# Kernel optimization log

Measured on AMD Instinct MI355X. Metric: run time of the kernel, lower is better.

The kernel has to match this reference:

```python
import jax, jax.numpy as jnp
import numpy as np

N_HEADS = 16
D_MODEL = 1024
D_HEAD = 64
MAX_SEQ_LEN = 1024


def setup_inputs() -> dict:
    key = jax.random.key(0)
    ks = jax.random.split(key, 7)
    std = np.sqrt(2.0 / (D_MODEL + D_HEAD)).astype(np.float32)
    hd = N_HEADS * D_HEAD
    # Weights stored as (in, out) so projection is x @ W (torch Linear y = x W^T).
    Wq = jax.random.normal(ks[0], (D_MODEL, hd), jnp.float32) * std
    Wk = jax.random.normal(ks[1], (D_MODEL, hd), jnp.float32) * std
    Wv = jax.random.normal(ks[2], (D_MODEL, hd), jnp.float32) * std
    Wo = jax.random.normal(ks[3], (hd, D_MODEL), jnp.float32) * (1.0 / np.sqrt(hd))
    bo = jnp.zeros((D_MODEL,), jnp.float32)
    rel_pos_bias = jax.random.normal(ks[4], (N_HEADS, MAX_SEQ_LEN), jnp.float32) * 0.02
    x = jax.random.normal(ks[5], (4, 1024, D_MODEL), jnp.float32)
    return {"x": x, "Wq": Wq, "Wk": Wk, "Wv": Wv, "Wo": Wo, "bo": bo,
            "rel_pos_bias": rel_pos_bias}


def _pos_bias(rel_pos_bias, T):
    # bias[h, i, j] = rel_pos_bias[h, MAX_SEQ_LEN - 1 - (i - j)] for j <= i, else 0
    i = jnp.arange(T)[:, None]
    j = jnp.arange(T)[None, :]
    idx = jnp.clip(MAX_SEQ_LEN - 1 - (i - j), 0, MAX_SEQ_LEN - 1)
    bias = rel_pos_bias[:, idx]                      # [H, T, T]
    return jnp.where((j <= i)[None], bias, 0.0)


def reference(x, Wq, Wk, Wv, Wo, bo, rel_pos_bias):
    B, T, _ = x.shape
    H, dh = N_HEADS, D_HEAD
    q = (x @ Wq).reshape(B, T, H, dh).transpose(0, 2, 1, 3)  # [B,H,T,dh]
    k = (x @ Wk).reshape(B, T, H, dh).transpose(0, 2, 1, 3)
    v = (x @ Wv).reshape(B, T, H, dh).transpose(0, 2, 1, 3)
    logits = jnp.einsum('bhqd,bhkd->bhqk', q, k)
    i = jnp.arange(T)[:, None]
    j = jnp.arange(T)[None, :]
    causal = jnp.where(j > i, -jnp.inf, 0.0)                 # [T,T]
    logits = logits + causal[None, None] + _pos_bias(rel_pos_bias, T)[None]
    logits = logits / dh                                     # note: /d_head, not sqrt
    probs = jax.nn.softmax(logits, axis=-1)
    out = jnp.einsum('bhqk,bhkd->bhqd', probs, v)            # [B,H,T,dh]
    out = out.transpose(0, 2, 1, 3).reshape(B, T, H * dh)
    return out @ Wo + bo
```

## Files before the change

kernel.cpp:

```cpp
#include <hip/hip_runtime.h>
#include <math.h>

#define BATCH 4
#define SEQ   1024
#define DM    1024
#define NH    16
#define DH    64
#define BT    (BATCH*SEQ)

typedef _Float16 f16x8 __attribute__((ext_vector_type(8)));
typedef _Float16 f16x4 __attribute__((ext_vector_type(4)));
typedef float    f32x4 __attribute__((ext_vector_type(4)));

#define GLL16(ldsdst, gsrc) \
  __builtin_amdgcn_global_load_lds((const __attribute__((address_space(1))) void*)(gsrc), \
                                   (__attribute__((address_space(3))) void*)(ldsdst), 16, 0, 0)

__global__ __launch_bounds__(256) void cvt_x(const float* __restrict__ x,
                                             _Float16* __restrict__ xh, int nquads)
{
    int i = blockIdx.x * blockDim.x + threadIdx.x;
    for (; i < nquads; i += gridDim.x * blockDim.x) {
        float4 f = ((const float4*)x)[i];
        f16x4 h;
        h[0] = (_Float16)f.x; h[1] = (_Float16)f.y;
        h[2] = (_Float16)f.z; h[3] = (_Float16)f.w;
        ((f16x4*)xh)[i] = h;
    }
}

__global__ __launch_bounds__(256) void cvt_wT(
    const float* __restrict__ W0, const float* __restrict__ W1,
    const float* __restrict__ W2, const float* __restrict__ W3,
    _Float16* __restrict__ T0, _Float16* __restrict__ T1,
    _Float16* __restrict__ T2, _Float16* __restrict__ T3)
{
    __shared__ _Float16 tile[64][72];
    const int z = blockIdx.z;
    const float* W = (z == 0) ? W0 : (z == 1) ? W1 : (z == 2) ? W2 : W3;
    _Float16*    T = (z == 0) ? T0 : (z == 1) ? T1 : (z == 2) ? T2 : T3;
    const int n0 = blockIdx.x * 64;
    const int k0 = blockIdx.y * 64;
    const int tid = threadIdx.x;
#pragma unroll
    for (int p = 0; p < 4; ++p) {
        int r = (tid >> 4) + p * 16;
        int c = (tid & 15) * 4;
        float4 f = *(const float4*)&W[(size_t)(k0 + r) * DM + n0 + c];
        f16x4 h;
        h[0] = (_Float16)f.x; h[1] = (_Float16)f.y;
        h[2] = (_Float16)f.z; h[3] = (_Float16)f.w;
        *(f16x4*)&tile[r][c] = h;
    }
    __syncthreads();
#pragma unroll
    for (int p = 0; p < 2; ++p) {
        int nr = (tid >> 3) + p * 32;
        int kc = (tid & 7) * 8;
        f16x8 vv;
#pragma unroll
        for (int i = 0; i < 8; ++i) vv[i] = tile[kc + i][nr];
        *(f16x8*)&T[(size_t)(n0 + nr) * DM + k0 + kc] = vv;
    }
}

template<int MODE>
__global__ __launch_bounds__(256) void gemm_mfma(
    const _Float16* __restrict__ A,
    const _Float16* __restrict__ B0, const _Float16* __restrict__ B1,
    const _Float16* __restrict__ B2,
    void* __restrict__ o0, void* __restrict__ o1, void* __restrict__ o2,
    const float* __restrict__ bias)
{
    __shared__ _Float16 As[128 * 32];
    __shared__ _Float16 Bs[128 * 32];

    const int tid = threadIdx.x;
    const int w   = tid >> 6;
    const int ln  = tid & 63;
    const int l15 = ln & 15;
    const int lg  = ln >> 4;
    const int wr  = w >> 1;
    const int wc  = w & 1;
    const int which = MODE ? (blockIdx.x >> 3) : 0;
    const int nl  = (blockIdx.x & 7) * 128;
    const int m0  = blockIdx.y * 128;

    const _Float16* Bt = (which == 0) ? B0 : (which == 1 ? B1 : B2);

    const int srow = ln >> 2;
    const int scol = (ln & 3) * 8;
    const _Float16* ga = A  + (size_t)(m0 + w * 32 + srow) * DM + scol;
    const _Float16* gb = Bt + (size_t)(nl + w * 32 + srow) * DM + scol;
    _Float16* la0 = &As[(w * 32 +  0) * 32];
    _Float16* la1 = &As[(w * 32 + 16) * 32];
    _Float16* lb0 = &Bs[(w * 32 +  0) * 32];
    _Float16* lb1 = &Bs[(w * 32 + 16) * 32];

    f32x4 acc[4][4];
#pragma unroll
    for (int i = 0; i < 4; ++i)
#pragma unroll
        for (int j = 0; j < 4; ++j) acc[i][j] = (f32x4){0.f, 0.f, 0.f, 0.f};

    for (int k0 = 0; k0 < DM; k0 += 32) {
        GLL16(la0, ga + k0);
        GLL16(la1, ga + k0 + (size_t)16 * DM);
        GLL16(lb0, gb + k0);
        GLL16(lb1, gb + k0 + (size_t)16 * DM);
        __syncthreads();

        f16x8 af[4], bf[4];
#pragma unroll
        for (int i = 0; i < 4; ++i)
            af[i] = *(const f16x8*)&As[(wr * 64 + i * 16 + l15) * 32 + lg * 8];
#pragma unroll
        for (int j = 0; j < 4; ++j)
            bf[j] = *(const f16x8*)&Bs[(wc * 64 + j * 16 + l15) * 32 + lg * 8];
#pragma unroll
        for (int i = 0; i < 4; ++i)
#pragma unroll
            for (int j = 0; j < 4; ++j)
                acc[i][j] = __builtin_amdgcn_mfma_f32_16x16x32_f16(af[i], bf[j], acc[i][j], 0, 0, 0);
        __syncthreads();
    }

    if (MODE == 1) {
        _Float16* outp = (which == 0) ? (_Float16*)o0
                        : (which == 1) ? (_Float16*)o1 : (_Float16*)o2;
        const float scale = (which == 0) ? 0.015625f : 1.0f;
#pragma unroll
        for (int i = 0; i < 4; ++i)
#pragma unroll
            for (int j = 0; j < 4; ++j) {
                int n  = nl + wc * 64 + j * 16 + l15;
                int hh = n >> 6, d = n & 63;
#pragma unroll
                for (int r = 0; r < 4; ++r) {
                    int m  = m0 + wr * 64 + i * 16 + lg * 4 + r;
                    int b_ = m >> 10, t_ = m & 1023;
                    outp[(((size_t)(b_ * NH + hh)) * SEQ + t_) * DH + d] =
                        (_Float16)(acc[i][j][r] * scale);
                }
            }
    } else {
        float* outp = (float*)o0;
#pragma unroll
        for (int i = 0; i < 4; ++i)
#pragma unroll
            for (int j = 0; j < 4; ++j) {
                int n = nl + wc * 64 + j * 16 + l15;
                float bz = bias[n];
#pragma unroll
                for (int r = 0; r < 4; ++r) {
                    int m = m0 + wr * 64 + i * 16 + lg * 4 + r;
                    outp[(size_t)m * DM + n] = acc[i][j][r] + bz;
                }
            }
    }
}

__global__ __launch_bounds__(256) void vtranspose(const _Float16* __restrict__ V,
                                                  _Float16* __restrict__ Vt)
{
    __shared__ _Float16 tile[64][72];
    const int bh = blockIdx.y;
    const int t0 = blockIdx.x * 64;
    const int tid = threadIdx.x;
    const int r = tid >> 3;
    const int c = (tid & 7) * 8;
    const size_t base = (size_t)bh * (SEQ * DH);
#pragma unroll
    for (int p = 0; p < 2; ++p) {
        int row = r + p * 32;
        *(f16x8*)&tile[row][c] = *(const f16x8*)&V[base + (size_t)(t0 + row) * DH + c];
    }
    __syncthreads();
#pragma unroll
    for (int p = 0; p < 2; ++p) {
        int d = r + p * 32;
        f16x8 vv;
#pragma unroll
        for (int i = 0; i < 8; ++i) vv[i] = tile[c + i][d];
        *(f16x8*)&Vt[base + (size_t)d * SEQ + t0 + c] = vv;
    }
}

__global__ __launch_bounds__(512) void attn_mfma(
    const _Float16* __restrict__ Q,
    const _Float16* __restrict__ K,
    const _Float16* __restrict__ Vt,
    const float* __restrict__ rpb,
    _Float16* __restrict__ ao)
{
    const int pr  = blockIdx.x;
    const int bh  = blockIdx.y;
    const int b_  = bh >> 4;
    const int h_  = bh & 15;
    const int tid = threadIdx.x;
    const int w   = tid >> 6;
    const int ln  = tid & 63;
    const int l15 = ln & 15;
    const int lg  = ln >> 4;

    __shared__ _Float16 Pb[8][16][72];
    __shared__ float rpb2[1152];

    {
        float2 t = *(const float2*)&rpb[h_ * SEQ + tid * 2];
        t.x *= 0.015625f; t.y *= 0.015625f;
        *(float2*)&rpb2[tid * 2] = t;
        if (tid < 128) rpb2[1024 + tid] = -1e30f;
    }
    __syncthreads();

    const size_t qkb = (size_t)bh * (SEQ * DH);
    const int qt  = (w < 4) ? pr : (15 - pr);
    const int qr0 = qt * 64 + (w & 3) * 16;
    const int i_  = qr0 + l15;

    f16x8 qa0, qa1;
    {
        const _Float16* qp = Q + qkb + (size_t)i_ * DH + lg * 8;
        qa0 = *(const f16x8*)qp;
        qa1 = *(const f16x8*)(qp + 32);
    }
    f32x4 accT[4];
#pragma unroll
    for (int dt = 0; dt < 4; ++dt) accT[dt] = (f32x4){0.f, 0.f, 0.f, 0.f};
    float m = -INFINITY, l = 0.f;

#pragma unroll 1
    for (int kt = 0; kt <= qt; ++kt) {
        const _Float16* kp = K + qkb + (size_t)(kt * 64 + l15) * DH + lg * 8;
        f32x4 sv[4];
#pragma unroll
        for (int st = 0; st < 4; ++st) {
            f16x8 kb0 = *(const f16x8*)(kp + st * 16 * DH);
            f16x8 kb1 = *(const f16x8*)(kp + st * 16 * DH + 32);
            f32x4 z = (f32x4){0.f, 0.f, 0.f, 0.f};
            z = __builtin_amdgcn_mfma_f32_16x16x32_f16(kb0, qa0, z, 0, 0, 0);
            z = __builtin_amdgcn_mfma_f32_16x16x32_f16(kb1, qa1, z, 0, 0, 0);
            sv[st] = z;
        }
        const int bidx = 1023 - i_ + kt * 64 + lg * 4;
        float tmax = -INFINITY;
#pragma unroll
        for (int st = 0; st < 4; ++st)
#pragma unroll
            for (int r = 0; r < 4; ++r) {
                float v = sv[st][r] + rpb2[bidx + st * 16 + r];
                sv[st][r] = v;
                tmax = fmaxf(tmax, v);
            }
        tmax = fmaxf(tmax, __shfl_xor(tmax, 16));
        tmax = fmaxf(tmax, __shfl_xor(tmax, 32));
        float mn   = fmaxf(m, tmax);
        float corr = __expf(m - mn);
        m = mn;
        float ps = 0.f;
#pragma unroll
        for (int st = 0; st < 4; ++st)
#pragma unroll
            for (int r = 0; r < 4; ++r) {
                float p = __expf(sv[st][r] - mn);
                sv[st][r] = p;
                ps += p;
            }
        ps += __shfl_xor(ps, 16);
        ps += __shfl_xor(ps, 32);
        l = l * corr + ps;
#pragma unroll
        for (int dt = 0; dt < 4; ++dt) {
            accT[dt][0] *= corr; accT[dt][1] *= corr;
            accT[dt][2] *= corr; accT[dt][3] *= corr;
        }
#pragma unroll
        for (int st = 0; st < 4; ++st) {
            f16x4 pk;
            pk[0] = (_Float16)sv[st][0]; pk[1] = (_Float16)sv[st][1];
            pk[2] = (_Float16)sv[st][2]; pk[3] = (_Float16)sv[st][3];
            *(f16x4*)&Pb[w][l15][st * 16 + lg * 4] = pk;
        }
        f16x8 pf0 = *(const f16x8*)&Pb[w][l15][lg * 8];
        f16x8 pf1 = *(const f16x8*)&Pb[w][l15][32 + lg * 8];
        const _Float16* vp = Vt + qkb + (size_t)l15 * SEQ + kt * 64 + lg * 8;
#pragma unroll
        for (int dt = 0; dt < 4; ++dt) {
            f16x8 vb0 = *(const f16x8*)(vp + dt * 16 * SEQ);
            f16x8 vb1 = *(const f16x8*)(vp + dt * 16 * SEQ + 32);
            accT[dt] = __builtin_amdgcn_mfma_f32_16x16x32_f16(vb0, pf0, accT[dt], 0, 0, 0);
            accT[dt] = __builtin_amdgcn_mfma_f32_16x16x32_f16(vb1, pf1, accT[dt], 0, 0, 0);
        }
    }
    float inv = 1.f / l;
    _Float16* aop = ao + ((size_t)(b_ * SEQ + i_)) * DM + h_ * DH + lg * 4;
#pragma unroll
    for (int dt = 0; dt < 4; ++dt) {
        f16x4 o4;
        o4[0] = (_Float16)(accT[dt][0] * inv);
        o4[1] = (_Float16)(accT[dt][1] * inv);
        o4[2] = (_Float16)(accT[dt][2] * inv);
        o4[3] = (_Float16)(accT[dt][3] * inv);
        *(f16x4*)&aop[dt * 16] = o4;
    }
}

extern "C" void kernel_launch(void* const* d_in, const int* in_sizes, int n_in,
                              void* d_out, int out_size, void* d_ws, size_t ws_size,
                              hipStream_t stream)
{
    (void)in_sizes; (void)n_in; (void)out_size; (void)ws_size;
    const float* x   = (const float*)d_in[0];
    const float* Wq  = (const float*)d_in[1];
    const float* Wk  = (const float*)d_in[2];
    const float* Wv  = (const float*)d_in[3];
    const float* Wo  = (const float*)d_in[4];
    const float* bo  = (const float*)d_in[5];
    const float* rpb = (const float*)d_in[6];
    float* out = (float*)d_out;

    char* ws = (char*)d_ws;
    _Float16* xh  = (_Float16*)(ws);
    _Float16* q   = (_Float16*)(ws + (8u  << 20));
    _Float16* k   = (_Float16*)(ws + (16u << 20));
    _Float16* v   = (_Float16*)(ws + (24u << 20));
    _Float16* vt  = (_Float16*)(ws + (32u << 20));
    _Float16* aoh = (_Float16*)(ws + (40u << 20));
    _Float16* wqt = (_Float16*)(ws + (48u << 20));
    _Float16* wkt = (_Float16*)(ws + (50u << 20));
    _Float16* wvt = (_Float16*)(ws + (52u << 20));
    _Float16* wot = (_Float16*)(ws + (54u << 20));

    cvt_x<<<2048, 256, 0, stream>>>(x, xh, BT * DM / 4);
    cvt_wT<<<dim3(16, 16, 4), 256, 0, stream>>>(Wq, Wk, Wv, Wo, wqt, wkt, wvt, wot);
    gemm_mfma<1><<<dim3(24, 32), 256, 0, stream>>>(xh, wqt, wkt, wvt, q, k, v, nullptr);
    vtranspose<<<dim3(SEQ / 64, BATCH * NH), 256, 0, stream>>>(v, vt);
    attn_mfma<<<dim3(8, BATCH * NH), 512, 0, stream>>>(q, k, vt, rpb, aoh);
    gemm_mfma<0><<<dim3(8, 32), 256, 0, stream>>>(aoh, wot, nullptr, nullptr, out, nullptr, nullptr, bo);
}
```

Measured before the change: 216.1 us.

## Split key tiles across wave pairs and merge partial softmax states in LDS

Before, each block paired q-tile pr with q-tile 15-pr, but half the waves ran pr+1 key iterations and the other half ran 16-pr, so waves finished at very different times. Now every wave pair covers the same 16 query rows of both q-tiles and splits the key tiles by parity. Each wave therefore does about the same number of iterations, which is meant to remove the idle tail inside a block. The partial accumulators and the running max and sum are combined through LDS after one barrier. This adds LDS traffic and a sync, and the partial outputs are rounded to fp16 before the merge, which costs some precision.

```diff
diff --git a/kernel.cpp b/kernel.cpp
--- a/kernel.cpp
+++ b/kernel.cpp
@@ -199,12 +199,16 @@
     const int h_  = bh & 15;
     const int tid = threadIdx.x;
     const int w   = tid >> 6;
+    const int j   = w >> 1;
+    const int s   = w & 1;
     const int ln  = tid & 63;
     const int l15 = ln & 15;
     const int lg  = ln >> 4;
 
     __shared__ _Float16 Pb[8][16][72];
-    __shared__ float rpb2[1152];
+    __shared__ _Float16 part[2][4][64][18];
+    __shared__ float    mlb[2][4][64][3];
+    __shared__ float    rpb2[1152];
 
     {
         float2 t = *(const float2*)&rpb[h_ * SEQ + tid * 2];
@@ -215,94 +219,128 @@
     __syncthreads();
 
     const size_t qkb = (size_t)bh * (SEQ * DH);
-    const int qt  = (w < 4) ? pr : (15 - pr);
-    const int qr0 = qt * 64 + (w & 3) * 16;
-    const int i_  = qr0 + l15;
-
-    f16x8 qa0, qa1;
-    {
-        const _Float16* qp = Q + qkb + (size_t)i_ * DH + lg * 8;
-        qa0 = *(const f16x8*)qp;
-        qa1 = *(const f16x8*)(qp + 32);
-    }
-    f32x4 accT[4];
-#pragma unroll
-    for (int dt = 0; dt < 4; ++dt) accT[dt] = (f32x4){0.f, 0.f, 0.f, 0.f};
-    float m = -INFINITY, l = 0.f;
-
+
+    auto run = [&](int qt, f32x4 (&accT)[4], float& m, float& l) {
+        const int i_ = qt * 64 + j * 16 + l15;
+        f16x8 qa0, qa1;
+        {
+            const _Float16* qp = Q + qkb + (size_t)i_ * DH + lg * 8;
+            qa0 = *(const f16x8*)qp;
+            qa1 = *(const f16x8*)(qp + 32);
+        }
 #pragma unroll 1
-    for (int kt = 0; kt <= qt; ++kt) {
-        const _Float16* kp = K + qkb + (size_t)(kt * 64 + l15) * DH + lg * 8;
-        f32x4 sv[4];
-#pragma unroll
-        for (int st = 0; st < 4; ++st) {
-            f16x8 kb0 = *(const f16x8*)(kp + st * 16 * DH);
-            f16x8 kb1 = *(const f16x8*)(kp + st * 16 * DH + 32);
-            f32x4 z = (f32x4){0.f, 0.f, 0.f, 0.f};
-            z = __builtin_amdgcn_mfma_f32_16x16x32_f16(kb0, qa0, z, 0, 0, 0);
-            z = __builtin_amdgcn_mfma_f32_16x16x32_f16(kb1, qa1, z, 0, 0, 0);
-            sv[st] = z;
+        for (int kt = s; kt <= qt; kt += 2) {
+            const _Float16* kp = K + qkb + (size_t)(kt * 64 + l15) * DH + lg * 8;
+            f32x4 sv[4];
+#pragma unroll
+            for (int st = 0; st < 4; ++st) {
+                f16x8 kb0 = *(const f16x8*)(kp + st * 16 * DH);
+                f16x8 kb1 = *(const f16x8*)(kp + st * 16 * DH + 32);
+                f32x4 z = (f32x4){0.f, 0.f, 0.f, 0.f};
+                z = __builtin_amdgcn_mfma_f32_16x16x32_f16(kb0, qa0, z, 0, 0, 0);
+                z = __builtin_amdgcn_mfma_f32_16x16x32_f16(kb1, qa1, z, 0, 0, 0);
+                sv[st] = z;
+            }
+            const int bidx = 1023 - i_ + kt * 64 + lg * 4;
+            float tmax = -INFINITY;
+#pragma unroll
+            for (int st = 0; st < 4; ++st)
+#pragma unroll
+                for (int r = 0; r < 4; ++r) {
+                    float v = sv[st][r] + rpb2[bidx + st * 16 + r];
+                    sv[st][r] = v;
+                    tmax = fmaxf(tmax, v);
+                }
+            tmax = fmaxf(tmax, __shfl_xor(tmax, 16));
+            tmax = fmaxf(tmax, __shfl_xor(tmax, 32));
+            float mn   = fmaxf(m, tmax);
+            float corr = __expf(m - mn);
+            m = mn;
+            float ps = 0.f;
+#pragma unroll
+            for (int st = 0; st < 4; ++st)
+#pragma unroll
+                for (int r = 0; r < 4; ++r) {
+                    float p = __expf(sv[st][r] - mn);
+                    sv[st][r] = p;
+                    ps += p;
+                }
+            ps += __shfl_xor(ps, 16);
+            ps += __shfl_xor(ps, 32);
+            l = l * corr + ps;
+#pragma unroll
+            for (int dt = 0; dt < 4; ++dt) {
+                accT[dt][0] *= corr; accT[dt][1] *= corr;
+                accT[dt][2] *= corr; accT[dt][3] *= corr;
+            }
+#pragma unroll
+            for (int st = 0; st < 4; ++st) {
+                f16x4 pk;
+                pk[0] = (_Float16)sv[st][0]; pk[1] = (_Float16)sv[st][1];
+                pk[2] = (_Float16)sv[st][2]; pk[3] = (_Float16)sv[st][3];
+                *(f16x4*)&Pb[w][l15][st * 16 + lg * 4] = pk;
+            }
+            f16x8 pf0 = *(const f16x8*)&Pb[w][l15][lg * 8];
+            f16x8 pf1 = *(const f16x8*)&Pb[w][l15][32 + lg * 8];
+            const _Float16* vp = Vt + qkb + (size_t)l15 * SEQ + kt * 64 + lg * 8;
+#pragma unroll
+            for (int dt = 0; dt < 4; ++dt) {
+                f16x8 vb0 = *(const f16x8*)(vp + dt * 16 * SEQ);
+                f16x8 vb1 = *(const f16x8*)(vp + dt * 16 * SEQ + 32);
+                accT[dt] = __builtin_amdgcn_mfma_f32_16x16x32_f16(vb0, pf0, accT[dt], 0, 0, 0);
+                accT[dt] = __builtin_amdgcn_mfma_f32_16x16x32_f16(vb1, pf1, accT[dt], 0, 0, 0);
+            }
         }
-        const int bidx = 1023 - i_ + kt * 64 + lg * 4;
-        float tmax = -INFINITY;
-#pragma unroll
-        for (int st = 0; st < 4; ++st)
-#pragma unroll
-            for (int r = 0; r < 4; ++r) {
-                float v = sv[st][r] + rpb2[bidx + st * 16 + r];
-                sv[st][r] = v;
-                tmax = fmaxf(tmax, v);
-            }
-        tmax = fmaxf(tmax, __shfl_xor(tmax, 16));
-        tmax = fmaxf(tmax, __shfl_xor(tmax, 32));
-        float mn   = fmaxf(m, tmax);
-        float corr = __expf(m - mn);
-        m = mn;
-        float ps = 0.f;
-#pragma unroll
-        for (int st = 0; st < 4; ++st)
-#pragma unroll
-            for (int r = 0; r < 4; ++r) {
-                float p = __expf(sv[st][r] - mn);
-                sv[st][r] = p;
-                ps += p;
-            }
-        ps += __shfl_xor(ps, 16);
-        ps += __shfl_xor(ps, 32);
-        l = l * corr + ps;
+    };
+
+    f32x4 accA[4], accB[4];
+    float mA = -INFINITY, lA = 0.f, mB = -INFINITY, lB = 0.f;
+#pragma unroll
+    for (int dt = 0; dt < 4; ++dt) {
+        accA[dt] = (f32x4){0.f, 0.f, 0.f, 0.f};
+        accB[dt] = (f32x4){0.f, 0.f, 0.f, 0.f};
+    }
+
+    run(pr, accA, mA, lA);
+    run(15 - pr, accB, mB, lB);
+
+    if (s == 1) {
 #pragma unroll
         for (int dt = 0; dt < 4; ++dt) {
-            accT[dt][0] *= corr; accT[dt][1] *= corr;
-            accT[dt][2] *= corr; accT[dt][3] *= corr;
+            f16x4 pa, pb_;
+#pragma unroll
+            for (int r = 0; r < 4; ++r) { pa[r] = (_Float16)accA[dt][r]; pb_[r] = (_Float16)accB[dt][r]; }
+            *(f16x4*)&part[0][j][ln][dt * 4] = pa;
+            *(f16x4*)&part[1][j][ln][dt * 4] = pb_;
         }
-#pragma unroll
-        for (int st = 0; st < 4; ++st) {
-            f16x4 pk;
-            pk[0] = (_Float16)sv[st][0]; pk[1] = (_Float16)sv[st][1];
-            pk[2] = (_Float16)sv[st][2]; pk[3] = (_Float16)sv[st][3];
-            *(f16x4*)&Pb[w][l15][st * 16 + lg * 4] = pk;
-        }
-        f16x8 pf0 = *(const f16x8*)&Pb[w][l15][lg * 8];
-        f16x8 pf1 = *(const f16x8*)&Pb[w][l15][32 + lg * 8];
-        const _Float16* vp = Vt + qkb + (size_t)l15 * SEQ + kt * 64 + lg * 8;
-#pragma unroll
-        for (int dt = 0; dt < 4; ++dt) {
-            f16x8 vb0 = *(const f16x8*)(vp + dt * 16 * SEQ);
-            f16x8 vb1 = *(const f16x8*)(vp + dt * 16 * SEQ + 32);
-            accT[dt] = __builtin_amdgcn_mfma_f32_16x16x32_f16(vb0, pf0, accT[dt], 0, 0, 0);
-            accT[dt] = __builtin_amdgcn_mfma_f32_16x16x32_f16(vb1, pf1, accT[dt], 0, 0, 0);
-        }
-    }
-    float inv = 1.f / l;
-    _Float16* aop = ao + ((size_t)(b_ * SEQ + i_)) * DM + h_ * DH + lg * 4;
-#pragma unroll
-    for (int dt = 0; dt < 4; ++dt) {
-        f16x4 o4;
-        o4[0] = (_Float16)(accT[dt][0] * inv);
-        o4[1] = (_Float16)(accT[dt][1] * inv);
-        o4[2] = (_Float16)(accT[dt][2] * inv);
-        o4[3] = (_Float16)(accT[dt][3] * inv);
-        *(f16x4*)&aop[dt * 16] = o4;
+        mlb[0][j][ln][0] = mA; mlb[0][j][ln][1] = lA;
+        mlb[1][j][ln][0] = mB; mlb[1][j][ln][1] = lB;
+    }
+    __syncthreads();
+
+    if (s == 0) {
+        auto merge = [&](int ji, int qt2, f32x4 (&accT)[4], float m, float l) {
+            float m1 = mlb[ji][j][ln][0];
+            float l1 = mlb[ji][j][ln][1];
+            float mm = fmaxf(m, m1);
+            float c0 = __expf(m - mm);
+            float c1 = __expf(m1 - mm);
+            float li = 1.f / (l * c0 + l1 * c1);
+            const int i2 = qt2 * 64 + j * 16 + l15;
+            _Float16* aop = ao + ((size_t)(b_ * SEQ + i2)) * DM + h_ * DH + lg * 4;
+#pragma unroll
+            for (int dt = 0; dt < 4; ++dt) {
+                f16x4 o4;
+#pragma unroll
+                for (int r = 0; r < 4; ++r) {
+                    float v = accT[dt][r] * c0 + (float)part[ji][j][ln][dt * 4 + r] * c1;
+                    o4[r] = (_Float16)(v * li);
+                }
+                *(f16x4*)&aop[dt * 16] = o4;
+            }
+        };
+        merge(0, pr, accA, mA, lA);
+        merge(1, 15 - pr, accB, mB, lB);
     }
 }
 
```

New measurement: 218.3 us. About the same (+1.0%).
